# Kernel optimization log

Measured on AMD Instinct MI355X. Metric: run time of the kernel, lower is better.

The kernel has to match this reference:

```python
import jax, jax.numpy as jnp
import numpy as np

N_NODES = 100000
N_EDGES = 300000
N_GRAPHS = 2048
F_ATOM = 40
D_IN = 128    # GINInputSize
D_HID = 256   # GINHiddenSize
D_OUT = 512   # FPSize
D_TASK = 1    # OutputSize


def _glorot(key, shape):
    fan_in, fan_out = shape[0], shape[1]
    lim = (6.0 / (fan_in + fan_out)) ** 0.5
    return jax.random.uniform(key, shape, jnp.float32, -lim, lim)


def setup_inputs() -> dict:
    key = jax.random.key(0)
    ks = jax.random.split(key, 16)
    inp = {
        'x': jax.random.normal(ks[0], (N_NODES, F_ATOM), jnp.float32),
        'edge_index': jax.random.randint(ks[1], (2, N_EDGES), 0, N_NODES, jnp.int64),
        'batch': jnp.sort(jax.random.randint(ks[2], (N_NODES,), 0, N_GRAPHS, jnp.int64)),
        # NodeFeatEmbed: MLP([F_ATOM, D_IN]) == single Linear (plain_last)
        'W_embed': _glorot(ks[3], (F_ATOM, D_IN)),
        'b_embed': jnp.zeros((D_IN,), jnp.float32),
        # GINConv eps per layer (train_eps=False -> 0.0 constants)
        'eps': jnp.zeros((3,), jnp.float32),
        # layer 0: MLP([D_IN, D_HID, D_HID])
        'W1_0': _glorot(ks[4], (D_IN, D_HID)),  'b1_0': jnp.zeros((D_HID,), jnp.float32),
        'W2_0': _glorot(ks[5], (D_HID, D_HID)), 'b2_0': jnp.zeros((D_HID,), jnp.float32),
        # layer 1: MLP([D_HID, D_HID, D_HID])
        'W1_1': _glorot(ks[6], (D_HID, D_HID)), 'b1_1': jnp.zeros((D_HID,), jnp.float32),
        'W2_1': _glorot(ks[7], (D_HID, D_HID)), 'b2_1': jnp.zeros((D_HID,), jnp.float32),
        # layer 2 (last, maps to out_channels=FPSize): MLP([D_HID, D_OUT, D_OUT])
        'W1_2': _glorot(ks[8], (D_HID, D_OUT)), 'b1_2': jnp.zeros((D_OUT,), jnp.float32),
        'W2_2': _glorot(ks[9], (D_OUT, D_OUT)), 'b2_2': jnp.zeros((D_OUT,), jnp.float32),
        # task head
        'W_task': _glorot(ks[10], (D_OUT, D_TASK)),
        'b_task': jnp.zeros((D_TASK,), jnp.float32),
    }
    return inp


def _gin_forward(x, edge_index, batch, W_embed, b_embed, eps, layers, W_task, b_task):
    src, dst = edge_index[0], edge_index[1]
    # NodeFeatEmbed
    h = x @ W_embed + b_embed                                    # [N, D_IN]
    n_layers = len(layers)
    for l, (W1, b1, W2, b2) in enumerate(layers):
        # GINConv: MLP((1+eps)*h + sum_{j->i} h_j)
        agg = jax.ops.segment_sum(h[src], dst, num_segments=N_NODES)
        z = (1.0 + eps[l]) * h + agg
        h = jax.nn.relu(z @ W1 + b1) @ W2 + b2
        if l < n_layers - 1:                                     # inter-layer act (not after last)
            h = jax.nn.relu(h)
    # global_add_pool readout
    pooled = jax.ops.segment_sum(h, batch, num_segments=N_GRAPHS)  # [G, D_OUT]
    return pooled @ W_task + b_task                               # [G, D_TASK]


def reference(x, edge_index, batch, W_embed, b_embed, eps,
              W1_0, b1_0, W2_0, b2_0,
              W1_1, b1_1, W2_1, b2_1,
              W1_2, b1_2, W2_2, b2_2,
              W_task, b_task):
    layers = [(W1_0, b1_0, W2_0, b2_0), (W1_1, b1_1, W2_1, b2_1), (W1_2, b1_2, W2_2, b2_2)]
    return _gin_forward(x, edge_index, batch, W_embed, b_embed, eps, layers, W_task, b_task)
```

## Files before the change

kernel.cpp:

```cpp
#include <hip/hip_runtime.h>

#define N_NODES 100000
#define E_EDGES 300000
#define N_GRAPHS 2048

typedef float  floatx4 __attribute__((ext_vector_type(4)));
typedef short  shortx8 __attribute__((ext_vector_type(8)));

__device__ __forceinline__ float bf2f(unsigned short u) {
  return __uint_as_float(((unsigned int)u) << 16);
}
__device__ __forceinline__ unsigned short f2bf(float f) {
  unsigned int u = __float_as_uint(f);
  u += 0x7FFFu + ((u >> 16) & 1u);
  return (unsigned short)(u >> 16);
}

__device__ __forceinline__ void cp16(const void* g, void* l) {
  __builtin_amdgcn_global_load_lds(
      (const __attribute__((address_space(1))) unsigned int*)g,
      (__attribute__((address_space(3))) unsigned int*)l, 16, 0, 0);
}

struct PrepArgs {
  const float* W[4];
  unsigned short* Wt[4];
  int K[4];
  int N[4];
  const float* We;
  const float* be;
  const float* W1_0;
  unsigned short* WfT;
  const float* W2_2;
  const float* b2_2;
  const float* wtask;
  float* w2v;
  float* c2;
  float* nodedot;
  float* out;
  const float* b_task;
};

__global__ __launch_bounds__(256)
void prep_kernel(PrepArgs a) {
  const int blk = blockIdx.x;
  if (blk < 320) {
    int z, b;
    if (blk < 64)       { z = 0; b = blk; }
    else if (blk < 128) { z = 1; b = blk - 64; }
    else if (blk < 192) { z = 2; b = blk - 128; }
    else                { z = 3; b = blk - 192; }
    const int K = a.K[z], N = a.N[z];
    const int nt = N / 32;
    const int kb = (b / nt) * 32, nb = (b % nt) * 32;
    __shared__ unsigned short tile[32][33];
    const float* W = a.W[z];
    unsigned short* Wt = a.Wt[z];
    const int tx = threadIdx.x & 31, ty = threadIdx.x >> 5;
    for (int r = ty; r < 32; r += 8)
      tile[r][tx] = f2bf(W[(size_t)(kb + r) * N + nb + tx]);
    __syncthreads();
    for (int r = ty; r < 32; r += 8)
      Wt[(size_t)(nb + r) * K + kb + tx] = tile[tx][r];
  } else if (blk < 361) {
    const int k = blk - 320;
    const int n = threadIdx.x;
    if (k < 40) {
      float s = 0.f;
      for (int j = 0; j < 128; j++) s = fmaf(a.We[k * 128 + j], a.W1_0[(size_t)j * 256 + n], s);
      a.WfT[n * 64 + k] = f2bf(s);
    } else {
      float s = 0.f;
      for (int j = 0; j < 128; j++) s = fmaf(a.be[j], a.W1_0[(size_t)j * 256 + n], s);
      a.WfT[n * 64 + 40] = f2bf(s);
      for (int kk = 41; kk < 64; kk++) a.WfT[n * 64 + kk] = 0;
    }
  } else if (blk < 490) {
    const int p = blk - 361;
    const int lane = threadIdx.x & 63;
    const int wave = threadIdx.x >> 6;
    if (p < 128) {
      const int k = p * 4 + wave;
      const float* row = a.W2_2 + (size_t)k * 512 + lane * 8;
      float4 a0 = *(const float4*)(row);
      float4 a1 = *(const float4*)(row + 4);
      float4 w0 = *(const float4*)(a.wtask + lane * 8);
      float4 w1 = *(const float4*)(a.wtask + lane * 8 + 4);
      float s = a0.x * w0.x + a0.y * w0.y + a0.z * w0.z + a0.w * w0.w +
                a1.x * w1.x + a1.y * w1.y + a1.z * w1.z + a1.w * w1.w;
#pragma unroll
      for (int off = 32; off > 0; off >>= 1) s += __shfl_down(s, off);
      if (lane == 0) a.w2v[k] = s;
    } else if (wave == 0) {
      float4 a0 = *(const float4*)(a.b2_2 + lane * 8);
      float4 a1 = *(const float4*)(a.b2_2 + lane * 8 + 4);
      float4 w0 = *(const float4*)(a.wtask + lane * 8);
      float4 w1 = *(const float4*)(a.wtask + lane * 8 + 4);
      float s = a0.x * w0.x + a0.y * w0.y + a0.z * w0.z + a0.w * w0.w +
                a1.x * w1.x + a1.y * w1.y + a1.z * w1.z + a1.w * w1.w;
#pragma unroll
      for (int off = 32; off > 0; off >>= 1) s += __shfl_down(s, off);
      if (lane == 0) *a.c2 = s;
    }
  } else if (blk < 881) {
    int i = (blk - 490) * 256 + threadIdx.x;
    if (i < N_NODES) a.nodedot[i] = 0.f;
  } else {
    int g = (blk - 881) * 256 + threadIdx.x;
    if (g < N_GRAPHS) a.out[g] = a.b_task[0];
  }
}

__global__ __launch_bounds__(256)
void zero_kernel(int* __restrict__ p, int n) {
  int i = blockIdx.x * 256 + threadIdx.x;
  if (i < n) p[i] = 0;
}

__global__ __launch_bounds__(256)
void hist_kernel(const int* __restrict__ ei, int* __restrict__ deg) {
  int e = blockIdx.x * 256 + threadIdx.x;
  if (e < E_EDGES) atomicAdd(&deg[ei[E_EDGES + e]], 1);
}

__global__ __launch_bounds__(256)
void scan_blk_kernel(const int* __restrict__ in, int* __restrict__ out,
                     int* __restrict__ blk_sums, int n_in, int n_out) {
  __shared__ int sm[256];
  const int t = threadIdx.x;
  const int base = blockIdx.x * 1024 + t * 4;
  int d0 = (base + 0 < n_in) ? in[base + 0] : 0;
  int d1 = (base + 1 < n_in) ? in[base + 1] : 0;
  int d2 = (base + 2 < n_in) ? in[base + 2] : 0;
  int d3 = (base + 3 < n_in) ? in[base + 3] : 0;
  int s = d0 + d1 + d2 + d3;
  sm[t] = s;
  __syncthreads();
  for (int off = 1; off < 256; off <<= 1) {
    int v = (t >= off) ? sm[t - off] : 0;
    __syncthreads();
    sm[t] += v;
    __syncthreads();
  }
  int excl = sm[t] - s;
  if (base + 0 < n_out) out[base + 0] = excl;
  if (base + 1 < n_out) out[base + 1] = excl + d0;
  if (base + 2 < n_out) out[base + 2] = excl + d0 + d1;
  if (base + 3 < n_out) out[base + 3] = excl + d0 + d1 + d2;
  if (t == 255 && blk_sums) blk_sums[blockIdx.x] = sm[255];
}

__global__ __launch_bounds__(256)
void scan_fix_kernel(int* __restrict__ row_ptr, const int* __restrict__ blk_off,
                     int* __restrict__ cursor) {
  int i = blockIdx.x * 256 + threadIdx.x;
  if (i <= N_NODES) {
    int v = row_ptr[i] + blk_off[i >> 10];
    row_ptr[i] = v;
    if (i < N_NODES) cursor[i] = v;
  }
}

__global__ __launch_bounds__(256)
void fill_kernel(const int* __restrict__ ei, int* __restrict__ cursor,
                 int* __restrict__ csr_src) {
  int e = blockIdx.x * 256 + threadIdx.x;
  if (e < E_EDGES) {
    int d = ei[E_EDGES + e];
    int slot = atomicAdd(&cursor[d], 1);
    csr_src[slot] = ei[e];
  }
}

__global__ __launch_bounds__(256)
void gatherx_kernel(const float* __restrict__ X, unsigned short* __restrict__ G,
                    const int* __restrict__ row_ptr, const int* __restrict__ csr,
                    const float* __restrict__ eps) {
  const int node = blockIdx.x * 4 + (threadIdx.x >> 6);
  const int lane = threadIdx.x & 63;
  const float sc = 1.0f + eps[0];
  const int e0 = row_ptr[node];
  const int e1 = row_ptr[node + 1];
  float acc = 0.f;
  if (lane < 40) {
    acc = sc * X[(size_t)node * 40 + lane];
    int e = e0;
    for (; e + 4 <= e1; e += 4) {
      int s0 = csr[e], s1 = csr[e + 1], s2 = csr[e + 2], s3 = csr[e + 3];
      float a0 = X[(size_t)s0 * 40 + lane];
      float a1 = X[(size_t)s1 * 40 + lane];
      float a2 = X[(size_t)s2 * 40 + lane];
      float a3 = X[(size_t)s3 * 40 + lane];
      acc += (a0 + a1) + (a2 + a3);
    }
    for (; e < e1; e++)
      acc += X[(size_t)csr[e] * 40 + lane];
  } else if (lane == 40) {
    acc = sc + (float)(e1 - e0);
  }
  G[(size_t)node * 64 + lane] = f2bf(acc);
}

__global__ __launch_bounds__(256)
void gather_kernel(const unsigned short* __restrict__ H, unsigned short* __restrict__ Z,
                   const int* __restrict__ row_ptr, const int* __restrict__ csr,
                   const float* __restrict__ eps, int l) {
  const int node = blockIdx.x * 4 + (threadIdx.x >> 6);
  const int lane = threadIdx.x & 63;
  const float sc = 1.0f + eps[l];
  uint2 hv = *(const uint2*)(H + (size_t)node * 256 + lane * 4);
  float acc[4];
  acc[0] = sc * bf2f((unsigned short)(hv.x & 0xFFFF));
  acc[1] = sc * bf2f((unsigned short)(hv.x >> 16));
  acc[2] = sc * bf2f((unsigned short)(hv.y & 0xFFFF));
  acc[3] = sc * bf2f((unsigned short)(hv.y >> 16));
  const int e0 = row_ptr[node];
  const int e1 = row_ptr[node + 1];
  int e = e0;
  for (; e + 2 <= e1; e += 2) {
    int s0 = csr[e], s1 = csr[e + 1];
    uint2 a = *(const uint2*)(H + (size_t)s0 * 256 + lane * 4);
    uint2 b = *(const uint2*)(H + (size_t)s1 * 256 + lane * 4);
    acc[0] += bf2f((unsigned short)(a.x & 0xFFFF)) + bf2f((unsigned short)(b.x & 0xFFFF));
    acc[1] += bf2f((unsigned short)(a.x >> 16))    + bf2f((unsigned short)(b.x >> 16));
    acc[2] += bf2f((unsigned short)(a.y & 0xFFFF)) + bf2f((unsigned short)(b.y & 0xFFFF));
    acc[3] += bf2f((unsigned short)(a.y >> 16))    + bf2f((unsigned short)(b.y >> 16));
  }
  if (e < e1) {
    int s0 = csr[e];
    uint2 a = *(const uint2*)(H + (size_t)s0 * 256 + lane * 4);
    acc[0] += bf2f((unsigned short)(a.x & 0xFFFF));
    acc[1] += bf2f((unsigned short)(a.x >> 16));
    acc[2] += bf2f((unsigned short)(a.y & 0xFFFF));
    acc[3] += bf2f((unsigned short)(a.y >> 16));
  }
  unsigned short z[4] = {f2bf(acc[0]), f2bf(acc[1]), f2bf(acc[2]), f2bf(acc[3])};
  *(uint2*)(Z + (size_t)node * 256 + lane * 4) = *(uint2*)z;
}

template <int K1>
__global__ __launch_bounds__(256, 2)
void fused_mlp_kernel(const unsigned short* __restrict__ A,
                      const unsigned short* __restrict__ W1t,
                      const float* __restrict__ b1,
                      const unsigned short* __restrict__ W2t,
                      const float* __restrict__ b2,
                      unsigned short* __restrict__ H,
                      int M) {
  constexpr int ACH = K1 / 8;
  constexpr int ZP = (64 * ACH) / 256;
  constexpr int NT1 = K1 / 32;

  __shared__ unsigned short Bs[2][256 * 32];
  __shared__ unsigned short Ts[64 * 256];

  const int m0 = blockIdx.x * 64;
  const int tid = threadIdx.x;
  const int lane = tid & 63;
  const int wave = tid >> 6;
  const int fr = lane & 15;
  const int fq = lane >> 4;
  const int wn = wave * 64;

#pragma unroll
  for (int p = 0; p < ZP; p++) {
    int slot = p * 256 + tid;
    int row = slot / ACH;
    int cs = slot % ACH;
    int cg = cs ^ (row & 7);
    int grow = m0 + row;
    if (grow >= M) grow = M - 1;
    cp16(A + (size_t)grow * K1 + cg * 8, Ts + (size_t)(p * 256 + wn) * 8);
  }

  const int bn_ = tid >> 2;
  const int bc_ = tid & 3;
  const unsigned short* srcW1[4];
  const unsigned short* srcW2[4];
#pragma unroll
  for (int p = 0; p < 4; p++) {
    int n = p * 64 + bn_;
    int sw = (bc_ ^ ((n >> 1) & 3)) << 3;
    srcW1[p] = W1t + (size_t)n * K1 + sw;
    srcW2[p] = W2t + (size_t)n * 256 + sw;
  }

  int offB[4];
#pragma unroll
  for (int j = 0; j < 4; j++) {
    int n = wn + j * 16 + fr;
    offB[j] = n * 32 + ((fq ^ ((n >> 1) & 3)) << 3);
  }

#pragma unroll
  for (int p = 0; p < 4; p++)
    cp16(srcW1[p], &Bs[0][(size_t)(p * 256 + wn) * 8]);

  floatx4 acc[4][4];
#pragma unroll
  for (int i = 0; i < 4; i++)
#pragma unroll
    for (int j = 0; j < 4; j++) acc[i][j] = (floatx4){0.f, 0.f, 0.f, 0.f};

  __syncthreads();
  int buf = 0;

  for (int t = 0; t < NT1; t++) {
    if (t + 1 < NT1) {
#pragma unroll
      for (int p = 0; p < 4; p++)
        cp16(srcW1[p] + (t + 1) * 32, &Bs[buf ^ 1][(size_t)(p * 256 + wn) * 8]);
    } else {
#pragma unroll
      for (int p = 0; p < 4; p++)
        cp16(srcW2[p], &Bs[buf ^ 1][(size_t)(p * 256 + wn) * 8]);
    }
    shortx8 af[4], bv[4];
    const int kc = t * 4;
#pragma unroll
    for (int i = 0; i < 4; i++) {
      int row = i * 16 + fr;
      af[i] = *(const shortx8*)&Ts[row * K1 + (((kc + fq) ^ (fr & 7)) << 3)];
    }
#pragma unroll
    for (int j = 0; j < 4; j++) bv[j] = *(const shortx8*)&Bs[buf][offB[j]];
#pragma unroll
    for (int i = 0; i < 4; i++)
#pragma unroll
      for (int j = 0; j < 4; j++)
        acc[i][j] = __builtin_amdgcn_mfma_f32_16x16x32_bf16(af[i], bv[j], acc[i][j], 0, 0, 0);
    __syncthreads();
    buf ^= 1;
  }

#pragma unroll
  for (int j = 0; j < 4; j++) {
    int col = wn + j * 16 + fr;
    float bb = b1[col];
    int cgc = col >> 3, c7 = col & 7;
#pragma unroll
    for (int i = 0; i < 4; i++)
#pragma unroll
      for (int r = 0; r < 4; r++) {
        int row = i * 16 + fq * 4 + r;
        float v = fmaxf(acc[i][j][r] + bb, 0.f);
        Ts[row * 256 + (((cgc ^ (row & 7)) << 3) | c7)] = f2bf(v);
        acc[i][j][r] = 0.f;
      }
  }
  __syncthreads();

  for (int t = 0; t < 8; t++) {
    if (t + 1 < 8) {
#pragma unroll
      for (int p = 0; p < 4; p++)
        cp16(srcW2[p] + (t + 1) * 32, &Bs[buf ^ 1][(size_t)(p * 256 + wn) * 8]);
    }
    shortx8 af[4], bv[4];
    const int kc = t * 4;
#pragma unroll
    for (int i = 0; i < 4; i++) {
      int row = i * 16 + fr;
      af[i] = *(const shortx8*)&Ts[row * 256 + (((kc + fq) ^ (fr & 7)) << 3)];
    }
#pragma unroll
    for (int j = 0; j < 4; j++) bv[j] = *(const shortx8*)&Bs[buf][offB[j]];
#pragma unroll
    for (int i = 0; i < 4; i++)
#pragma unroll
      for (int j = 0; j < 4; j++)
        acc[i][j] = __builtin_amdgcn_mfma_f32_16x16x32_bf16(af[i], bv[j], acc[i][j], 0, 0, 0);
    __syncthreads();
    buf ^= 1;
  }

#pragma unroll
  for (int j = 0; j < 4; j++) {
    int col = wn + j * 16 + fr;
    float bb = b2[col];
    int cgc = col >> 3, c7 = col & 7;
#pragma unroll
    for (int i = 0; i < 4; i++)
#pragma unroll
      for (int r = 0; r < 4; r++) {
        int row = i * 16 + fq * 4 + r;
        float v = fmaxf(acc[i][j][r] + bb, 0.f);
        Ts[row * 256 + (((cgc ^ (row & 7)) << 3) | c7)] = f2bf(v);
      }
  }
  __syncthreads();
  const int r2 = tid >> 5;
  const int cg2 = tid & 31;
#pragma unroll
  for (int p = 0; p < 8; p++) {
    int row = p * 8 + r2;
    int grow = m0 + row;
    if (grow < M) {
      uint4 v = *(const uint4*)&Ts[row * 256 + ((cg2 ^ (row & 7)) << 3)];
      *(uint4*)&H[(size_t)grow * 256 + cg2 * 8] = v;
    }
  }
}

__global__ __launch_bounds__(256, 2)
void fused_dot_kernel(const unsigned short* __restrict__ A,
                      const unsigned short* __restrict__ W1t,
                      const float* __restrict__ b1,
                      const float* __restrict__ w2v,
                      float* __restrict__ nodedot4, int M) {
  __shared__ unsigned short Bs[2][256 * 32];
  __shared__ unsigned short Ts[64 * 256];

  const int m0 = blockIdx.x * 64;
  const int tid = threadIdx.x;
  const int lane = tid & 63;
  const int wave = tid >> 6;
  const int fr = lane & 15;
  const int fq = lane >> 4;
  const int wn = wave * 64;

#pragma unroll
  for (int p = 0; p < 8; p++) {
    int slot = p * 256 + tid;
    int row = slot >> 5;
    int cs = slot & 31;
    int cg = cs ^ (row & 7);
    int grow = m0 + row;
    if (grow >= M) grow = M - 1;
    cp16(A + (size_t)grow * 256 + cg * 8, Ts + (size_t)(p * 256 + wn) * 8);
  }

  const int bn_ = tid >> 2;
  const int bc_ = tid & 3;
  const unsigned short* srcW[4];
#pragma unroll
  for (int p = 0; p < 4; p++) {
    int n = p * 64 + bn_;
    srcW[p] = W1t + (size_t)n * 256 + ((bc_ ^ ((n >> 1) & 3)) << 3);
  }
  int offB[4];
#pragma unroll
  for (int j = 0; j < 4; j++) {
    int n = wn + j * 16 + fr;
    offB[j] = n * 32 + ((fq ^ ((n >> 1) & 3)) << 3);
  }

#pragma unroll
  for (int p = 0; p < 4; p++)
    cp16(srcW[p], &Bs[0][(size_t)(p * 256 + wn) * 8]);

  float pd[4][4];
#pragma unroll
  for (int i = 0; i < 4; i++)
#pragma unroll
    for (int r = 0; r < 4; r++) pd[i][r] = 0.f;

  floatx4 acc[4][4];
#pragma unroll
  for (int i = 0; i < 4; i++)
#pragma unroll
    for (int j = 0; j < 4; j++) acc[i][j] = (floatx4){0.f, 0.f, 0.f, 0.f};

  __syncthreads();
  int buf = 0;

  for (int s = 0; s < 16; s++) {
    int ns = s + 1;
    if (ns < 16) {
      const size_t off = (size_t)(ns >> 3) * 65536 + (size_t)(ns & 7) * 32;
#pragma unroll
      for (int p = 0; p < 4; p++)
        cp16(srcW[p] + off, &Bs[buf ^ 1][(size_t)(p * 256 + wn) * 8]);
    }
    shortx8 af[4], bv[4];
    const int kc = (s & 7) * 4;
#pragma unroll
    for (int i = 0; i < 4; i++) {
      int row = i * 16 + fr;
      af[i] = *(const shortx8*)&Ts[row * 256 + (((kc + fq) ^ (fr & 7)) << 3)];
    }
#pragma unroll
    for (int j = 0; j < 4; j++) bv[j] = *(const shortx8*)&Bs[buf][offB[j]];
#pragma unroll
    for (int i = 0; i < 4; i++)
#pragma unroll
      for (int j = 0; j < 4; j++)
        acc[i][j] = __builtin_amdgcn_mfma_f32_16x16x32_bf16(af[i], bv[j], acc[i][j], 0, 0, 0);
    __syncthreads();
    buf ^= 1;

    if ((s & 7) == 7) {
      const int nh = s >> 3;
#pragma unroll
      for (int j = 0; j < 4; j++) {
        int col = nh * 256 + wn + j * 16 + fr;
        float bb = b1[col];
        float wv = w2v[col];
#pragma unroll
        for (int i = 0; i < 4; i++)
#pragma unroll
          for (int r = 0; r < 4; r++) {
            pd[i][r] += fmaxf(acc[i][j][r] + bb, 0.f) * wv;
            acc[i][j][r] = 0.f;
          }
      }
    }
  }

#pragma unroll
  for (int i = 0; i < 4; i++)
#pragma unroll
    for (int r = 0; r < 4; r++) {
      float s = pd[i][r];
#pragma unroll
      for (int off = 1; off < 16; off <<= 1) s += __shfl_xor(s, off);
      if (fr == 0) {
        int row = m0 + i * 16 + fq * 4 + r;
        if (row < M) nodedot4[(size_t)wave * N_NODES + row] = s;
      }
    }
}

__global__ __launch_bounds__(256)
void pool_kernel(const float* __restrict__ nodedot4, const int* __restrict__ batch,
                 float* __restrict__ out, const float* __restrict__ c2p) {
  const int i = blockIdx.x * 256 + threadIdx.x;
  if (i >= N_NODES) return;
  const int lane = threadIdx.x & 63;
  const float c2 = *c2p;
  float v = (nodedot4[i] + nodedot4[N_NODES + i]) +
            (nodedot4[2 * N_NODES + i] + nodedot4[3 * N_NODES + i]) + c2;
  const int g = batch[i];
  float s = v;
#pragma unroll
  for (int off = 1; off < 64; off <<= 1) {
    float u = __shfl_up(s, off);
    int gu = __shfl_up(g, off);
    if (lane >= off && gu == g) s += u;
  }
  bool last = (i == N_NODES - 1) || (batch[i + 1] != g) || (lane == 63);
  if (last) unsafeAtomicAdd(&out[g], s);
}

extern "C" void kernel_launch(void* const* d_in, const int* in_sizes, int n_in,
                              void* d_out, int out_size, void* d_ws, size_t ws_size,
                              hipStream_t stream) {
  const float* x       = (const float*)d_in[0];
  const int*   ei      = (const int*)d_in[1];
  const int*   batch   = (const int*)d_in[2];
  const float* W_embed = (const float*)d_in[3];
  const float* b_embed = (const float*)d_in[4];
  const float* eps     = (const float*)d_in[5];
  const float* W1[3] = {(const float*)d_in[6],  (const float*)d_in[10], (const float*)d_in[14]};
  const float* B1[3] = {(const float*)d_in[7],  (const float*)d_in[11], (const float*)d_in[15]};
  const float* W2[3] = {(const float*)d_in[8],  (const float*)d_in[12], (const float*)d_in[16]};
  const float* B2[3] = {(const float*)d_in[9],  (const float*)d_in[13], (const float*)d_in[17]};
  const float* W_task = (const float*)d_in[18];
  const float* b_task = (const float*)d_in[19];
  float* out = (float*)d_out;

  const size_t OFF_ND4 = 51200000;
  const size_t OFF_RZ  = 102400000;
  const size_t OFF_AUX = 153600000;
  if (ws_size < OFF_AUX + 4000000) return;
  unsigned short* RH = (unsigned short*)d_ws;
  float* nodedot4 = (float*)((char*)d_ws + OFF_ND4);
  unsigned short* RZ = (unsigned short*)((char*)d_ws + OFF_RZ);
  char* aux = (char*)d_ws + OFF_AUX;
  int* row_ptr  = (int*)(aux);
  int* cursor   = (int*)(aux + 400016);
  int* csr_src  = (int*)(aux + 800016);
  int* blk_sums = (int*)(aux + 2000016);
  int* blk_off  = (int*)(aux + 2000416);
  float* nodedot = (float*)(aux + 2000816);
  unsigned short* WT = (unsigned short*)(aux + 2400832);
  float* w2v = (float*)(aux + 3200832);
  float* c2  = (float*)(aux + 3202880);
  unsigned short* WfT    = WT;
  unsigned short* Wt2_0  = WT + 32768;
  unsigned short* Wt1_1  = WT + 98304;
  unsigned short* Wt2_1  = WT + 163840;
  unsigned short* Wt1_2  = WT + 229376;

  PrepArgs pa;
  pa.W[0] = W2[0]; pa.Wt[0] = Wt2_0; pa.K[0] = 256; pa.N[0] = 256;
  pa.W[1] = W1[1]; pa.Wt[1] = Wt1_1; pa.K[1] = 256; pa.N[1] = 256;
  pa.W[2] = W2[1]; pa.Wt[2] = Wt2_1; pa.K[2] = 256; pa.N[2] = 256;
  pa.W[3] = W1[2]; pa.Wt[3] = Wt1_2; pa.K[3] = 256; pa.N[3] = 512;
  pa.We = W_embed; pa.be = b_embed; pa.W1_0 = W1[0]; pa.WfT = WfT;
  pa.W2_2 = W2[2]; pa.b2_2 = B2[2]; pa.wtask = W_task; pa.w2v = w2v; pa.c2 = c2;
  pa.nodedot = nodedot; pa.out = out; pa.b_task = b_task;
  prep_kernel<<<889, 256, 0, stream>>>(pa);

  zero_kernel<<<(N_NODES + 255) / 256, 256, 0, stream>>>(cursor, N_NODES);
  hist_kernel<<<(E_EDGES + 255) / 256, 256, 0, stream>>>(ei, cursor);
  scan_blk_kernel<<<98, 256, 0, stream>>>(cursor, row_ptr, blk_sums, N_NODES, N_NODES + 1);
  scan_blk_kernel<<<1, 256, 0, stream>>>(blk_sums, blk_off, nullptr, 98, 98);
  scan_fix_kernel<<<(N_NODES + 256) / 256, 256, 0, stream>>>(row_ptr, blk_off, cursor);
  fill_kernel<<<(E_EDGES + 255) / 256, 256, 0, stream>>>(ei, cursor, csr_src);

  const int FB = (N_NODES + 63) / 64;

  gatherx_kernel<<<N_NODES / 4, 256, 0, stream>>>(x, RZ, row_ptr, csr_src, eps);
  fused_mlp_kernel<64><<<FB, 256, 0, stream>>>(RZ, WfT, B1[0], Wt2_0, B2[0], RH, N_NODES);

  gather_kernel<<<N_NODES / 4, 256, 0, stream>>>(RH, RZ, row_ptr, csr_src, eps, 1);
  fused_mlp_kernel<256><<<FB, 256, 0, stream>>>(RZ, Wt1_1, B1[1], Wt2_1, B2[1], RH, N_NODES);

  gather_kernel<<<N_NODES / 4, 256, 0, stream>>>(RH, RZ, row_ptr, csr_src, eps, 2);
  fused_dot_kernel<<<FB, 256, 0, stream>>>(RZ, Wt1_2, B1[2], w2v, nodedot4, N_NODES);

  pool_kernel<<<(N_NODES + 255) / 256, 256, 0, stream>>>(nodedot4, batch, out, c2);
}
```

Baseline: 394.1 us.

## Fuse neighbor gather into MLP kernels for layers 1 and 2

```diff
diff --git a/kernel.cpp b/kernel.cpp
--- a/kernel.cpp
+++ b/kernel.cpp
@@ -20,6 +20,61 @@
   __builtin_amdgcn_global_load_lds(
       (const __attribute__((address_space(1))) unsigned int*)g,
       (__attribute__((address_space(3))) unsigned int*)l, 16, 0, 0);
+}
+
+__device__ __forceinline__ void acc8(float* a, uint4 v) {
+  a[0] += bf2f((unsigned short)(v.x & 0xFFFF));
+  a[1] += bf2f((unsigned short)(v.x >> 16));
+  a[2] += bf2f((unsigned short)(v.y & 0xFFFF));
+  a[3] += bf2f((unsigned short)(v.y >> 16));
+  a[4] += bf2f((unsigned short)(v.z & 0xFFFF));
+  a[5] += bf2f((unsigned short)(v.z >> 16));
+  a[6] += bf2f((unsigned short)(v.w & 0xFFFF));
+  a[7] += bf2f((unsigned short)(v.w >> 16));
+}
+
+__device__ __forceinline__ void gather_stage(
+    const unsigned short* __restrict__ H, const int* __restrict__ row_ptr,
+    const int* __restrict__ csr, float sc, int m0, int M,
+    unsigned short* Ts, int tid) {
+  const int c = tid & 31;
+  const int r0 = tid >> 5;
+#pragma unroll
+  for (int p = 0; p < 8; p++) {
+    const int row = r0 + p * 8;
+    int node = m0 + row;
+    if (node >= M) node = M - 1;
+    uint4 v = *(const uint4*)(H + (size_t)node * 256 + c * 8);
+    float a0[8], a1[8];
+    a0[0] = sc * bf2f((unsigned short)(v.x & 0xFFFF));
+    a0[1] = sc * bf2f((unsigned short)(v.x >> 16));
+    a0[2] = sc * bf2f((unsigned short)(v.y & 0xFFFF));
+    a0[3] = sc * bf2f((unsigned short)(v.y >> 16));
+    a0[4] = sc * bf2f((unsigned short)(v.z & 0xFFFF));
+    a0[5] = sc * bf2f((unsigned short)(v.z >> 16));
+    a0[6] = sc * bf2f((unsigned short)(v.w & 0xFFFF));
+    a0[7] = sc * bf2f((unsigned short)(v.w >> 16));
+#pragma unroll
+    for (int k = 0; k < 8; k++) a1[k] = 0.f;
+    const int e0 = row_ptr[node];
+    const int e1 = row_ptr[node + 1];
+    int e = e0;
+    for (; e + 2 <= e1; e += 2) {
+      int s0 = csr[e], s1 = csr[e + 1];
+      uint4 u0 = *(const uint4*)(H + (size_t)s0 * 256 + c * 8);
+      uint4 u1 = *(const uint4*)(H + (size_t)s1 * 256 + c * 8);
+      acc8(a0, u0);
+      acc8(a1, u1);
+    }
+    if (e < e1) {
+      uint4 u0 = *(const uint4*)(H + (size_t)csr[e] * 256 + c * 8);
+      acc8(a0, u0);
+    }
+    unsigned short z[8];
+#pragma unroll
+    for (int k = 0; k < 8; k++) z[k] = f2bf(a0[k] + a1[k]);
+    *(uint4*)&Ts[row * 256 + ((c ^ (row & 7)) << 3)] = *(const uint4*)z;
+  }
 }
 
 struct PrepArgs {
@@ -112,12 +167,6 @@
 }
 
 __global__ __launch_bounds__(256)
-void zero_kernel(int* __restrict__ p, int n) {
-  int i = blockIdx.x * 256 + threadIdx.x;
-  if (i < n) p[i] = 0;
-}
-
-__global__ __launch_bounds__(256)
 void hist_kernel(const int* __restrict__ ei, int* __restrict__ deg) {
   int e = blockIdx.x * 256 + threadIdx.x;
   if (e < E_EDGES) atomicAdd(&deg[ei[E_EDGES + e]], 1);
@@ -201,43 +250,6 @@
   G[(size_t)node * 64 + lane] = f2bf(acc);
 }
 
-__global__ __launch_bounds__(256)
-void gather_kernel(const unsigned short* __restrict__ H, unsigned short* __restrict__ Z,
-                   const int* __restrict__ row_ptr, const int* __restrict__ csr,
-                   const float* __restrict__ eps, int l) {
-  const int node = blockIdx.x * 4 + (threadIdx.x >> 6);
-  const int lane = threadIdx.x & 63;
-  const float sc = 1.0f + eps[l];
-  uint2 hv = *(const uint2*)(H + (size_t)node * 256 + lane * 4);
-  float acc[4];
-  acc[0] = sc * bf2f((unsigned short)(hv.x & 0xFFFF));
-  acc[1] = sc * bf2f((unsigned short)(hv.x >> 16));
-  acc[2] = sc * bf2f((unsigned short)(hv.y & 0xFFFF));
-  acc[3] = sc * bf2f((unsigned short)(hv.y >> 16));
-  const int e0 = row_ptr[node];
-  const int e1 = row_ptr[node + 1];
-  int e = e0;
-  for (; e + 2 <= e1; e += 2) {
-    int s0 = csr[e], s1 = csr[e + 1];
-    uint2 a = *(const uint2*)(H + (size_t)s0 * 256 + lane * 4);
-    uint2 b = *(const uint2*)(H + (size_t)s1 * 256 + lane * 4);
-    acc[0] += bf2f((unsigned short)(a.x & 0xFFFF)) + bf2f((unsigned short)(b.x & 0xFFFF));
-    acc[1] += bf2f((unsigned short)(a.x >> 16))    + bf2f((unsigned short)(b.x >> 16));
-    acc[2] += bf2f((unsigned short)(a.y & 0xFFFF)) + bf2f((unsigned short)(b.y & 0xFFFF));
-    acc[3] += bf2f((unsigned short)(a.y >> 16))    + bf2f((unsigned short)(b.y >> 16));
-  }
-  if (e < e1) {
-    int s0 = csr[e];
-    uint2 a = *(const uint2*)(H + (size_t)s0 * 256 + lane * 4);
-    acc[0] += bf2f((unsigned short)(a.x & 0xFFFF));
-    acc[1] += bf2f((unsigned short)(a.x >> 16));
-    acc[2] += bf2f((unsigned short)(a.y & 0xFFFF));
-    acc[3] += bf2f((unsigned short)(a.y >> 16));
-  }
-  unsigned short z[4] = {f2bf(acc[0]), f2bf(acc[1]), f2bf(acc[2]), f2bf(acc[3])};
-  *(uint2*)(Z + (size_t)node * 256 + lane * 4) = *(uint2*)z;
-}
-
 template <int K1>
 __global__ __launch_bounds__(256, 2)
 void fused_mlp_kernel(const unsigned short* __restrict__ A,
@@ -403,11 +415,16 @@
 }
 
 __global__ __launch_bounds__(256, 2)
-void fused_dot_kernel(const unsigned short* __restrict__ A,
-                      const unsigned short* __restrict__ W1t,
-                      const float* __restrict__ b1,
-                      const float* __restrict__ w2v,
-                      float* __restrict__ nodedot4, int M) {
+void fused_mlp_g_kernel(const unsigned short* __restrict__ Hin,
+                        const int* __restrict__ row_ptr,
+                        const int* __restrict__ csr,
+                        const float* __restrict__ eps, int l,
+                        const unsigned short* __restrict__ W1t,
+                        const float* __restrict__ b1,
+                        const unsigned short* __restrict__ W2t,
+                        const float* __restrict__ b2,
+                        unsigned short* __restrict__ Hout,
+                        int M) {
   __shared__ unsigned short Bs[2][256 * 32];
   __shared__ unsigned short Ts[64 * 256];
 
@@ -419,16 +436,155 @@
   const int fq = lane >> 4;
   const int wn = wave * 64;
 
+  const int bn_ = tid >> 2;
+  const int bc_ = tid & 3;
+  const unsigned short* srcW1[4];
+  const unsigned short* srcW2[4];
+#pragma unroll
+  for (int p = 0; p < 4; p++) {
+    int n = p * 64 + bn_;
+    int sw = (bc_ ^ ((n >> 1) & 3)) << 3;
+    srcW1[p] = W1t + (size_t)n * 256 + sw;
+    srcW2[p] = W2t + (size_t)n * 256 + sw;
+  }
+  int offB[4];
+#pragma unroll
+  for (int j = 0; j < 4; j++) {
+    int n = wn + j * 16 + fr;
+    offB[j] = n * 32 + ((fq ^ ((n >> 1) & 3)) << 3);
+  }
+
+#pragma unroll
+  for (int p = 0; p < 4; p++)
+    cp16(srcW1[p], &Bs[0][(size_t)(p * 256 + wn) * 8]);
+
+  gather_stage(Hin, row_ptr, csr, 1.0f + eps[l], m0, M, Ts, tid);
+
+  floatx4 acc[4][4];
+#pragma unroll
+  for (int i = 0; i < 4; i++)
+#pragma unroll
+    for (int j = 0; j < 4; j++) acc[i][j] = (floatx4){0.f, 0.f, 0.f, 0.f};
+
+  __syncthreads();
+  int buf = 0;
+
+  for (int t = 0; t < 8; t++) {
+    if (t + 1 < 8) {
+#pragma unroll
+      for (int p = 0; p < 4; p++)
+        cp16(srcW1[p] + (t + 1) * 32, &Bs[buf ^ 1][(size_t)(p * 256 + wn) * 8]);
+    } else {
+#pragma unroll
+      for (int p = 0; p < 4; p++)
+        cp16(srcW2[p], &Bs[buf ^ 1][(size_t)(p * 256 + wn) * 8]);
+    }
+    shortx8 af[4], bv[4];
+    const int kc = t * 4;
+#pragma unroll
+    for (int i = 0; i < 4; i++) {
+      int row = i * 16 + fr;
+      af[i] = *(const shortx8*)&Ts[row * 256 + (((kc + fq) ^ (fr & 7)) << 3)];
+    }
+#pragma unroll
+    for (int j = 0; j < 4; j++) bv[j] = *(const shortx8*)&Bs[buf][offB[j]];
+#pragma unroll
+    for (int i = 0; i < 4; i++)
+#pragma unroll
+      for (int j = 0; j < 4; j++)
+        acc[i][j] = __builtin_amdgcn_mfma_f32_16x16x32_bf16(af[i], bv[j], acc[i][j], 0, 0, 0);
+    __syncthreads();
+    buf ^= 1;
+  }
+
+#pragma unroll
+  for (int j = 0; j < 4; j++) {
+    int col = wn + j * 16 + fr;
+    float bb = b1[col];
+    int cgc = col >> 3, c7 = col & 7;
+#pragma unroll
+    for (int i = 0; i < 4; i++)
+#pragma unroll
+      for (int r = 0; r < 4; r++) {
+        int row = i * 16 + fq * 4 + r;
+        float v = fmaxf(acc[i][j][r] + bb, 0.f);
+        Ts[row * 256 + (((cgc ^ (row & 7)) << 3) | c7)] = f2bf(v);
+        acc[i][j][r] = 0.f;
+      }
+  }
+  __syncthreads();
+
+  for (int t = 0; t < 8; t++) {
+    if (t + 1 < 8) {
+#pragma unroll
+      for (int p = 0; p < 4; p++)
+        cp16(srcW2[p] + (t + 1) * 32, &Bs[buf ^ 1][(size_t)(p * 256 + wn) * 8]);
+    }
+    shortx8 af[4], bv[4];
+    const int kc = t * 4;
+#pragma unroll
+    for (int i = 0; i < 4; i++) {
+      int row = i * 16 + fr;
+      af[i] = *(const shortx8*)&Ts[row * 256 + (((kc + fq) ^ (fr & 7)) << 3)];
+    }
+#pragma unroll
+    for (int j = 0; j < 4; j++) bv[j] = *(const shortx8*)&Bs[buf][offB[j]];
+#pragma unroll
+    for (int i = 0; i < 4; i++)
+#pragma unroll
+      for (int j = 0; j < 4; j++)
+        acc[i][j] = __builtin_amdgcn_mfma_f32_16x16x32_bf16(af[i], bv[j], acc[i][j], 0, 0, 0);
+    __syncthreads();
+    buf ^= 1;
+  }
+
+#pragma unroll
+  for (int j = 0; j < 4; j++) {
+    int col = wn + j * 16 + fr;
+    float bb = b2[col];
+    int cgc = col >> 3, c7 = col & 7;
+#pragma unroll
+    for (int i = 0; i < 4; i++)
+#pragma unroll
+      for (int r = 0; r < 4; r++) {
+        int row = i * 16 + fq * 4 + r;
+        float v = fmaxf(acc[i][j][r] + bb, 0.f);
+        Ts[row * 256 + (((cgc ^ (row & 7)) << 3) | c7)] = f2bf(v);
+      }
+  }
+  __syncthreads();
+  const int r2 = tid >> 5;
+  const int cg2 = tid & 31;
 #pragma unroll
   for (int p = 0; p < 8; p++) {
-    int slot = p * 256 + tid;
-    int row = slot >> 5;
-    int cs = slot & 31;
-    int cg = cs ^ (row & 7);
+    int row = p * 8 + r2;
     int grow = m0 + row;
-    if (grow >= M) grow = M - 1;
-    cp16(A + (size_t)grow * 256 + cg * 8, Ts + (size_t)(p * 256 + wn) * 8);
-  }
+    if (grow < M) {
+      uint4 v = *(const uint4*)&Ts[row * 256 + ((cg2 ^ (row & 7)) << 3)];
+      *(uint4*)&Hout[(size_t)grow * 256 + cg2 * 8] = v;
+    }
+  }
+}
+
+__global__ __launch_bounds__(256, 2)
+void fused_dot_g_kernel(const unsigned short* __restrict__ Hin,
+                        const int* __restrict__ row_ptr,
+                        const int* __restrict__ csr,
+                        const float* __restrict__ eps, int l,
+                        const unsigned short* __restrict__ W1t,
+                        const float* __restrict__ b1,
+                        const float* __restrict__ w2v,
+                        float* __restrict__ nodedot4, int M) {
+  __shared__ unsigned short Bs[2][256 * 32];
+  __shared__ unsigned short Ts[64 * 256];
+
+  const int m0 = blockIdx.x * 64;
+  const int tid = threadIdx.x;
+  const int lane = tid & 63;
+  const int wave = tid >> 6;
+  const int fr = lane & 15;
+  const int fq = lane >> 4;
+  const int wn = wave * 64;
 
   const int bn_ = tid >> 2;
   const int bc_ = tid & 3;
@@ -448,6 +604,8 @@
 #pragma unroll
   for (int p = 0; p < 4; p++)
     cp16(srcW[p], &Bs[0][(size_t)(p * 256 + wn) * 8]);
+
+  gather_stage(Hin, row_ptr, csr, 1.0f + eps[l], m0, M, Ts, tid);
 
   float pd[4][4];
 #pragma unroll
@@ -572,7 +730,6 @@
   int* csr_src  = (int*)(aux + 800016);
   int* blk_sums = (int*)(aux + 2000016);
   int* blk_off  = (int*)(aux + 2000416);
-  float* nodedot = (float*)(aux + 2000816);
   unsigned short* WT = (unsigned short*)(aux + 2400832);
   float* w2v = (float*)(aux + 3200832);
   float* c2  = (float*)(aux + 3202880);
@@ -589,10 +746,10 @@
   pa.W[3] = W1[2]; pa.Wt[3] = Wt1_2; pa.K[3] = 256; pa.N[3] = 512;
   pa.We = W_embed; pa.be = b_embed; pa.W1_0 = W1[0]; pa.WfT = WfT;
   pa.W2_2 = W2[2]; pa.b2_2 = B2[2]; pa.wtask = W_task; pa.w2v = w2v; pa.c2 = c2;
-  pa.nodedot = nodedot; pa.out = out; pa.b_task = b_task;
+  pa.nodedot = (float*)cursor;
+  pa.out = out; pa.b_task = b_task;
   prep_kernel<<<889, 256, 0, stream>>>(pa);
 
-  zero_kernel<<<(N_NODES + 255) / 256, 256, 0, stream>>>(cursor, N_NODES);
   hist_kernel<<<(E_EDGES + 255) / 256, 256, 0, stream>>>(ei, cursor);
   scan_blk_kernel<<<98, 256, 0, stream>>>(cursor, row_ptr, blk_sums, N_NODES, N_NODES + 1);
   scan_blk_kernel<<<1, 256, 0, stream>>>(blk_sums, blk_off, nullptr, 98, 98);
@@ -604,11 +761,11 @@
   gatherx_kernel<<<N_NODES / 4, 256, 0, stream>>>(x, RZ, row_ptr, csr_src, eps);
   fused_mlp_kernel<64><<<FB, 256, 0, stream>>>(RZ, WfT, B1[0], Wt2_0, B2[0], RH, N_NODES);
 
-  gather_kernel<<<N_NODES / 4, 256, 0, stream>>>(RH, RZ, row_ptr, csr_src, eps, 1);
-  fused_mlp_kernel<256><<<FB, 256, 0, stream>>>(RZ, Wt1_1, B1[1], Wt2_1, B2[1], RH, N_NODES);
-
-  gather_kernel<<<N_NODES / 4, 256, 0, stream>>>(RH, RZ, row_ptr, csr_src, eps, 2);
-  fused_dot_kernel<<<FB, 256, 0, stream>>>(RZ, Wt1_2, B1[2], w2v, nodedot4, N_NODES);
+  fused_mlp_g_kernel<<<FB, 256, 0, stream>>>(RH, row_ptr, csr_src, eps, 1,
+                                             Wt1_1, B1[1], Wt2_1, B2[1], RZ, N_NODES);
+
+  fused_dot_g_kernel<<<FB, 256, 0, stream>>>(RZ, row_ptr, csr_src, eps, 2,
+                                             Wt1_2, B1[2], w2v, nodedot4, N_NODES);
 
   pool_kernel<<<(N_NODES + 255) / 256, 256, 0, stream>>>(nodedot4, batch, out, c2);
 }
```

New measurement: 434.0 us. 10.1% more time.
